# Performance work log

Measured on AMD Instinct MI355X. Metric: run time of the kernel, lower is better.

The kernel has to match this reference:

```python
import jax, jax.numpy as jnp
import numpy as np

N_NODES = 100000

def graph_conv(x, edge_index, w_root, w_rel, b):
    # PyG GraphConv (aggr='add'): out = aggr(x_j) @ W_rel + b + x @ W_root
    src, dst = edge_index[0], edge_index[1]
    msgs = x[src]                                   # [E, F_in] gather
    agg = jax.ops.segment_sum(msgs, dst, num_segments=N_NODES)  # [N, F_in] scatter-add
    return agg @ w_rel + b + x @ w_root             # [N, F_out]


def setup_inputs() -> dict:
    key = jax.random.key(0)
    ks = jax.random.split(key, 12)
    E = 1600000
    return {
        "x": jax.random.normal(ks[0], (N_NODES, 16), dtype=jnp.float32),
        "edge_index": jax.random.randint(ks[1], (2, E), 0, N_NODES, dtype=jnp.int64),
        "w_root1": jax.random.normal(ks[2], (16, 32), dtype=jnp.float32) * 0.1,
        "w_rel1": jax.random.normal(ks[3], (16, 32), dtype=jnp.float32) * 0.1,
        "b1": jax.random.normal(ks[4], (32,), dtype=jnp.float32) * 0.1,
        "w_root2": jax.random.normal(ks[5], (32, 64), dtype=jnp.float32) * 0.1,
        "w_rel2": jax.random.normal(ks[6], (32, 64), dtype=jnp.float32) * 0.1,
        "b2": jax.random.normal(ks[7], (64,), dtype=jnp.float32) * 0.1,
        "fc1_w": jax.random.normal(ks[8], (64, 32), dtype=jnp.float32) * 0.1,
        "fc1_b": jax.random.normal(ks[9], (32,), dtype=jnp.float32) * 0.1,
        "fc2_w": jax.random.normal(ks[10], (32, 16), dtype=jnp.float32) * 0.1,
        "fc2_b": jax.random.normal(ks[11], (16,), dtype=jnp.float32) * 0.1,
    }


def reference(x, edge_index, w_root1, w_rel1, b1, w_root2, w_rel2, b2,
              fc1_w, fc1_b, fc2_w, fc2_b):
    h = jax.nn.relu(graph_conv(x, edge_index, w_root1, w_rel1, b1))   # [N, 32]
    h = jax.nn.relu(graph_conv(h, edge_index, w_root2, w_rel2, b2))   # [N, 64]
    h = jax.nn.relu(h @ fc1_w + fc1_b)                                 # [N, 32]
    return h @ fc2_w + fc2_b                                           # [N, 16]
```

## Files before the change

### kernel.cpp

```cpp
#include <hip/hip_runtime.h>

#define F4E(v,i) ((i)==0?(v).x:((i)==1?(v).y:((i)==2?(v).z:(v).w)))

#define CHUNK 8192

__device__ inline float4 shfl4b(float4 v, int src) {
    float4 r;
    r.x = __shfl(v.x, src, 4); r.y = __shfl(v.y, src, 4);
    r.z = __shfl(v.z, src, 4); r.w = __shfl(v.w, src, 4);
    return r;
}

__global__ __launch_bounds__(512) void k_bhist(
    const int* __restrict__ ei, int* __restrict__ bhist, int E, int NB)
{
    __shared__ int cnt[512];
    int t = threadIdx.x;
    cnt[t] = 0;
    __syncthreads();
    int base = blockIdx.x * CHUNK;
#pragma unroll
    for (int i = 0; i < 16; ++i) {
        int e = base + i * 512 + t;
        if (e < E) {
            int dst = ei[E + e];
            atomicAdd(&cnt[dst >> 8], 1);
        }
    }
    __syncthreads();
    if (t < NB && cnt[t]) atomicAdd(&bhist[t], cnt[t]);
}

__global__ __launch_bounds__(512) void k_bscan(
    const int* __restrict__ bhist, int* __restrict__ bstart,
    int* __restrict__ gcursor, int NB, int E)
{
    __shared__ int s[512];
    int t = threadIdx.x;
    int v0 = (t < NB) ? bhist[t] : 0;
    s[t] = v0;
    __syncthreads();
    for (int off = 1; off < 512; off <<= 1) {
        int v = (t >= off) ? s[t - off] : 0;
        __syncthreads();
        s[t] += v;
        __syncthreads();
    }
    if (t < NB) { int ex = s[t] - v0; bstart[t] = ex; gcursor[t] = ex; }
    if (t == 0) bstart[NB] = E;
}

__global__ __launch_bounds__(512) void k_partition(
    const int* __restrict__ ei, int* __restrict__ gcursor,
    int* __restrict__ epack, int E)
{
    __shared__ int cnt[512], sc[512], lbase[512], gbase[512], lcnt[512];
    __shared__ int stage[CHUNK];
    __shared__ unsigned short stageb[CHUNK];
    int t = threadIdx.x;
    cnt[t] = 0; lcnt[t] = 0;
    __syncthreads();

    int base = blockIdx.x * CHUNK;
    int pk[16], bb[16];
#pragma unroll
    for (int i = 0; i < 16; ++i) {
        int e = base + i * 512 + t;
        if (e < E) {
            int src = ei[e], dst = ei[E + e];
            pk[i] = (src << 8) | (dst & 255);
            bb[i] = dst >> 8;
            atomicAdd(&cnt[bb[i]], 1);
        } else bb[i] = -1;
    }
    __syncthreads();

    int v0 = cnt[t];
    sc[t] = v0;
    __syncthreads();
    for (int off = 1; off < 512; off <<= 1) {
        int v = (t >= off) ? sc[t - off] : 0;
        __syncthreads();
        sc[t] += v;
        __syncthreads();
    }
    lbase[t] = sc[t] - v0;
    if (v0 > 0) gbase[t] = atomicAdd(&gcursor[t], v0);
    __syncthreads();

#pragma unroll
    for (int i = 0; i < 16; ++i) {
        if (bb[i] >= 0) {
            int loc = atomicAdd(&lcnt[bb[i]], 1);
            int slot = lbase[bb[i]] + loc;
            stage[slot] = pk[i];
            stageb[slot] = (unsigned short)bb[i];
        }
    }
    __syncthreads();

    int m = min(CHUNK, E - base);
#pragma unroll
    for (int i = 0; i < 16; ++i) {
        int slot = i * 512 + t;
        if (slot < m) {
            int b = stageb[slot];
            epack[gbase[b] + (slot - lbase[b])] = stage[slot];
        }
    }
}

__global__ __launch_bounds__(256) void k_sort(
    const int* __restrict__ bstart, const int* __restrict__ epack,
    int* __restrict__ rs, int* __restrict__ esorted, int N, int E)
{
    __shared__ int hist[256], cur[256], sc[256];
    int t = threadIdx.x;
    int b = blockIdx.x;
    int s0 = bstart[b], s1 = bstart[b + 1];
    hist[t] = 0;
    __syncthreads();
    for (int e = s0 + t; e < s1; e += 256)
        atomicAdd(&hist[epack[e] & 255], 1);
    __syncthreads();

    int v0 = hist[t];
    sc[t] = v0;
    __syncthreads();
    for (int off = 1; off < 256; off <<= 1) {
        int v = (t >= off) ? sc[t - off] : 0;
        __syncthreads();
        sc[t] += v;
        __syncthreads();
    }
    int excl = sc[t] - v0;
    cur[t] = excl;
    int node = (b << 8) + t;
    if (node < N) rs[node] = s0 + excl;
    if (b == 0 && t == 0) rs[N] = E;
    __syncthreads();

    for (int e = s0 + t; e < s1; e += 256) {
        int pk = epack[e];
        int dlo = pk & 255;
        int pos = s0 + atomicAdd(&cur[dlo], 1);
        esorted[pos] = ((unsigned)pk) >> 8;
    }
}

__global__ __launch_bounds__(256) void k_g1f(
    const float* __restrict__ x, const int* __restrict__ rs,
    const int* __restrict__ esrc,
    const float* __restrict__ wroot, const float* __restrict__ wrel,
    const float* __restrict__ bias, float* __restrict__ h1, int N)
{
    __shared__ float4 s_wr[128], s_wl[128], s_b[8];
    int t = threadIdx.x;
    if (t < 128) {
        s_wr[t] = reinterpret_cast<const float4*>(wroot)[t];
        s_wl[t] = reinterpret_cast<const float4*>(wrel)[t];
    }
    if (t < 8) s_b[t] = reinterpret_cast<const float4*>(bias)[t];
    __syncthreads();

    int tid = blockIdx.x * 256 + t;
    int n = tid >> 2, p = tid & 3;
    if (n >= N) return;
    int s0 = rs[n], s1 = rs[n + 1];
    float4 g = make_float4(0.f, 0.f, 0.f, 0.f);
    int e = s0;
    for (; e + 1 < s1; e += 2) {
        int src0 = esrc[e], src1 = esrc[e + 1];
        float4 v0 = *reinterpret_cast<const float4*>(x + (size_t)src0 * 16 + p * 4);
        float4 v1 = *reinterpret_cast<const float4*>(x + (size_t)src1 * 16 + p * 4);
        g.x += v0.x + v1.x; g.y += v0.y + v1.y;
        g.z += v0.z + v1.z; g.w += v0.w + v1.w;
    }
    if (e < s1) {
        int src0 = esrc[e];
        float4 v0 = *reinterpret_cast<const float4*>(x + (size_t)src0 * 16 + p * 4);
        g.x += v0.x; g.y += v0.y; g.z += v0.z; g.w += v0.w;
    }
    float4 a = *reinterpret_cast<const float4*>(x + (size_t)n * 16 + p * 4);

    int jb = p * 2;
    float4 acc0 = s_b[jb], acc1 = s_b[jb + 1];
#pragma unroll
    for (int kc = 0; kc < 4; ++kc) {
        float4 a4 = shfl4b(a, kc);
        float4 g4 = shfl4b(g, kc);
#pragma unroll
        for (int kk = 0; kk < 4; ++kk) {
            float av = F4E(a4, kk), gv = F4E(g4, kk);
            int k = kc * 4 + kk;
            float4 wr0 = s_wr[k * 8 + jb], wr1 = s_wr[k * 8 + jb + 1];
            float4 wl0 = s_wl[k * 8 + jb], wl1 = s_wl[k * 8 + jb + 1];
            acc0.x += av * wr0.x + gv * wl0.x;
            acc0.y += av * wr0.y + gv * wl0.y;
            acc0.z += av * wr0.z + gv * wl0.z;
            acc0.w += av * wr0.w + gv * wl0.w;
            acc1.x += av * wr1.x + gv * wl1.x;
            acc1.y += av * wr1.y + gv * wl1.y;
            acc1.z += av * wr1.z + gv * wl1.z;
            acc1.w += av * wr1.w + gv * wl1.w;
        }
    }
    acc0.x = fmaxf(acc0.x, 0.f); acc0.y = fmaxf(acc0.y, 0.f);
    acc0.z = fmaxf(acc0.z, 0.f); acc0.w = fmaxf(acc0.w, 0.f);
    acc1.x = fmaxf(acc1.x, 0.f); acc1.y = fmaxf(acc1.y, 0.f);
    acc1.z = fmaxf(acc1.z, 0.f); acc1.w = fmaxf(acc1.w, 0.f);
    float4* o = reinterpret_cast<float4*>(h1 + (size_t)n * 32 + p * 8);
    o[0] = acc0; o[1] = acc1;
}

__global__ __launch_bounds__(256) void k_gather32(
    const float* __restrict__ x, const int* __restrict__ rs,
    const int* __restrict__ esrc, float* __restrict__ agg, int N)
{
    int tid = blockIdx.x * 256 + threadIdx.x;
    int n = tid >> 3, p = tid & 7;
    if (n >= N) return;
    int s0 = rs[n], s1 = rs[n + 1];
    float4 acc = make_float4(0.f, 0.f, 0.f, 0.f);
    int e = s0;
    for (; e + 1 < s1; e += 2) {
        int src0 = esrc[e], src1 = esrc[e + 1];
        float4 v0 = *reinterpret_cast<const float4*>(x + (size_t)src0 * 32 + p * 4);
        float4 v1 = *reinterpret_cast<const float4*>(x + (size_t)src1 * 32 + p * 4);
        acc.x += v0.x + v1.x; acc.y += v0.y + v1.y;
        acc.z += v0.z + v1.z; acc.w += v0.w + v1.w;
    }
    if (e < s1) {
        int src0 = esrc[e];
        float4 v0 = *reinterpret_cast<const float4*>(x + (size_t)src0 * 32 + p * 4);
        acc.x += v0.x; acc.y += v0.y; acc.z += v0.z; acc.w += v0.w;
    }
    *reinterpret_cast<float4*>(agg + (size_t)n * 32 + p * 4) = acc;
}

__global__ __launch_bounds__(256) void k_l2v2(
    const float* __restrict__ h1, const float* __restrict__ agg,
    const float* __restrict__ wroot, const float* __restrict__ wrel,
    const float* __restrict__ bias,
    const float* __restrict__ f1w, const float* __restrict__ f1b,
    const float* __restrict__ f2w, const float* __restrict__ f2b,
    float* __restrict__ out, int N)
{
    __shared__ float4 s_wr[512], s_wl[512], s_b[16];
    __shared__ float4 s_f1[512], s_f2[128], s_b1[8], s_b2[4];
    int t = threadIdx.x;
    for (int i = t; i < 512; i += 256) {
        s_wr[i] = reinterpret_cast<const float4*>(wroot)[i];
        s_wl[i] = reinterpret_cast<const float4*>(wrel)[i];
        s_f1[i] = reinterpret_cast<const float4*>(f1w)[i];
    }
    if (t < 128) s_f2[t] = reinterpret_cast<const float4*>(f2w)[t];
    if (t < 16) s_b[t]  = reinterpret_cast<const float4*>(bias)[t];
    if (t < 8)  s_b1[t] = reinterpret_cast<const float4*>(f1b)[t];
    if (t < 4)  s_b2[t] = reinterpret_cast<const float4*>(f2b)[t];
    __syncthreads();

    int gid = blockIdx.x * 256 + t;
    int n = gid >> 1, p = gid & 1;
    if (n >= N) return;
    const float4* xr = reinterpret_cast<const float4*>(h1 + (size_t)n * 32);
    const float4* ar = reinterpret_cast<const float4*>(agg + (size_t)n * 32);
    float4 X0 = xr[0], X1 = xr[1], X2 = xr[2], X3 = xr[3];
    float4 X4 = xr[4], X5 = xr[5], X6 = xr[6], X7 = xr[7];
    float4 G0 = ar[0], G1 = ar[1], G2 = ar[2], G3 = ar[3];
    float4 G4 = ar[4], G5 = ar[5], G6 = ar[6], G7 = ar[7];

    int jb = p * 8;
    float4 acc[8];
#pragma unroll
    for (int jc = 0; jc < 8; ++jc) acc[jc] = s_b[jb + jc];

#define L2STEP(Xc, Gc, kcv)                                          \
    {                                                                \
        _Pragma("unroll")                                            \
        for (int kk = 0; kk < 4; ++kk) {                             \
            float a = F4E(Xc, kk), g = F4E(Gc, kk);                  \
            int k = (kcv) * 4 + kk;                                  \
            _Pragma("unroll")                                        \
            for (int jc = 0; jc < 8; ++jc) {                         \
                float4 wr = s_wr[k * 16 + jb + jc];                  \
                float4 wl = s_wl[k * 16 + jb + jc];                  \
                acc[jc].x += a * wr.x + g * wl.x;                    \
                acc[jc].y += a * wr.y + g * wl.y;                    \
                acc[jc].z += a * wr.z + g * wl.z;                    \
                acc[jc].w += a * wr.w + g * wl.w;                    \
            }                                                        \
        }                                                            \
    }
    L2STEP(X0, G0, 0) L2STEP(X1, G1, 1) L2STEP(X2, G2, 2) L2STEP(X3, G3, 3)
    L2STEP(X4, G4, 4) L2STEP(X5, G5, 5) L2STEP(X6, G6, 6) L2STEP(X7, G7, 7)
#undef L2STEP

#pragma unroll
    for (int jc = 0; jc < 8; ++jc) {
        acc[jc].x = fmaxf(acc[jc].x, 0.f); acc[jc].y = fmaxf(acc[jc].y, 0.f);
        acc[jc].z = fmaxf(acc[jc].z, 0.f); acc[jc].w = fmaxf(acc[jc].w, 0.f);
    }

    float4 f[8];
    float4 z4 = make_float4(0.f, 0.f, 0.f, 0.f);
#pragma unroll
    for (int jc = 0; jc < 8; ++jc) f[jc] = p ? z4 : s_b1[jc];
#pragma unroll
    for (int kk = 0; kk < 32; ++kk) {
        float hv = F4E(acc[kk >> 2], kk & 3);
        int k = p * 32 + kk;
#pragma unroll
        for (int jc = 0; jc < 8; ++jc) {
            float4 w = s_f1[k * 8 + jc];
            f[jc].x += hv * w.x; f[jc].y += hv * w.y;
            f[jc].z += hv * w.z; f[jc].w += hv * w.w;
        }
    }
#pragma unroll
    for (int jc = 0; jc < 8; ++jc) {
        f[jc].x += __shfl_xor(f[jc].x, 1);
        f[jc].y += __shfl_xor(f[jc].y, 1);
        f[jc].z += __shfl_xor(f[jc].z, 1);
        f[jc].w += __shfl_xor(f[jc].w, 1);
        f[jc].x = fmaxf(f[jc].x, 0.f); f[jc].y = fmaxf(f[jc].y, 0.f);
        f[jc].z = fmaxf(f[jc].z, 0.f); f[jc].w = fmaxf(f[jc].w, 0.f);
    }

    int ob = p * 2;
    float4 o0 = s_b2[ob], o1 = s_b2[ob + 1];
#pragma unroll
    for (int k2 = 0; k2 < 32; ++k2) {
        float a = F4E(f[k2 >> 2], k2 & 3);
        float4 w0 = s_f2[k2 * 4 + ob], w1 = s_f2[k2 * 4 + ob + 1];
        o0.x += a * w0.x; o0.y += a * w0.y; o0.z += a * w0.z; o0.w += a * w0.w;
        o1.x += a * w1.x; o1.y += a * w1.y; o1.z += a * w1.z; o1.w += a * w1.w;
    }
    float4* o = reinterpret_cast<float4*>(out + (size_t)n * 16 + p * 8);
    o[0] = o0; o[1] = o1;
}

extern "C" void kernel_launch(void* const* d_in, const int* in_sizes, int n_in,
                              void* d_out, int out_size, void* d_ws, size_t ws_size,
                              hipStream_t stream)
{
    const float* x   = (const float*)d_in[0];
    const int*   ei  = (const int*)d_in[1];
    const float* wr1 = (const float*)d_in[2];
    const float* wl1 = (const float*)d_in[3];
    const float* b1  = (const float*)d_in[4];
    const float* wr2 = (const float*)d_in[5];
    const float* wl2 = (const float*)d_in[6];
    const float* b2  = (const float*)d_in[7];
    const float* f1w = (const float*)d_in[8];
    const float* f1b = (const float*)d_in[9];
    const float* f2w = (const float*)d_in[10];
    const float* f2b = (const float*)d_in[11];
    float* out = (float*)d_out;

    const int N  = in_sizes[0] / 16;
    const int E  = in_sizes[1] / 2;
    const int NB = (N + 255) >> 8;

    float* ws      = (float*)d_ws;
    float* h1      = ws;
    float* agg2    = ws + (size_t)N * 32;
    int*   esorted = (int*)(ws + (size_t)N * 64);
    int*   epack   = esorted + E;
    int*   rs      = epack + E;
    int*   bhist   = rs + N + 1;
    int*   bstart  = bhist + NB;
    int*   gcursor = bstart + NB + 1;

    hipMemsetAsync(bhist, 0, (size_t)NB * sizeof(int), stream);

    int nchunk = (E + CHUNK - 1) / CHUNK;
    int g_g1 = (N * 4 + 255) / 256;
    int g_g2 = (N * 8 + 255) / 256;
    int g_l2 = (N * 2 + 255) / 256;

    k_bhist    <<<nchunk, 512, 0, stream>>>(ei, bhist, E, NB);
    k_bscan    <<<1,      512, 0, stream>>>(bhist, bstart, gcursor, NB, E);
    k_partition<<<nchunk, 512, 0, stream>>>(ei, gcursor, epack, E);
    k_sort     <<<NB,     256, 0, stream>>>(bstart, epack, rs, esorted, N, E);

    k_g1f      <<<g_g1, 256, 0, stream>>>(x, rs, esorted, wr1, wl1, b1, h1, N);
    k_gather32 <<<g_g2, 256, 0, stream>>>(h1, rs, esorted, agg2, N);
    k_l2v2     <<<g_l2, 256, 0, stream>>>(h1, agg2, wr2, wl2, b2,
                                          f1w, f1b, f2w, f2b, out, N);
}
```

Measured before the change: 232.2 us.

## Fuse layer-2 gather with dense MLP tail and halve partition chunk size

Merges the layer-2 neighbor gather and the dense layer-2/fc1/fc2 kernel into one kernel with 8 threads per node. Each thread gathers a float4 slice of the aggregate, then shares the slices with shuffles for the GraphConv matmul. fc1 partial sums are reduced with an xor-shuffle tree across the 8 lanes, and the fc1 weights are stored in shared memory with a rotated layout to avoid bank conflicts. This removes the agg2 intermediate write and read plus one launch, at the cost of more shuffles and register pressure. Separately, the partition chunk size is halved so those kernels launch more blocks with fewer edges each.

```diff
diff --git a/kernel.cpp b/kernel.cpp
--- a/kernel.cpp
+++ b/kernel.cpp
@@ -2,7 +2,8 @@
 
 #define F4E(v,i) ((i)==0?(v).x:((i)==1?(v).y:((i)==2?(v).z:(v).w)))
 
-#define CHUNK 8192
+#define CHUNK 4096
+#define ITERS 8
 
 __device__ inline float4 shfl4b(float4 v, int src) {
     float4 r;
@@ -10,6 +11,12 @@
     r.z = __shfl(v.z, src, 4); r.w = __shfl(v.w, src, 4);
     return r;
 }
+__device__ inline float4 shfl8b(float4 v, int src) {
+    float4 r;
+    r.x = __shfl(v.x, src, 8); r.y = __shfl(v.y, src, 8);
+    r.z = __shfl(v.z, src, 8); r.w = __shfl(v.w, src, 8);
+    return r;
+}
 
 __global__ __launch_bounds__(512) void k_bhist(
     const int* __restrict__ ei, int* __restrict__ bhist, int E, int NB)
@@ -20,7 +27,7 @@
     __syncthreads();
     int base = blockIdx.x * CHUNK;
 #pragma unroll
-    for (int i = 0; i < 16; ++i) {
+    for (int i = 0; i < ITERS; ++i) {
         int e = base + i * 512 + t;
         if (e < E) {
             int dst = ei[E + e];
@@ -62,9 +69,9 @@
     __syncthreads();
 
     int base = blockIdx.x * CHUNK;
-    int pk[16], bb[16];
-#pragma unroll
-    for (int i = 0; i < 16; ++i) {
+    int pk[ITERS], bb[ITERS];
+#pragma unroll
+    for (int i = 0; i < ITERS; ++i) {
         int e = base + i * 512 + t;
         if (e < E) {
             int src = ei[e], dst = ei[E + e];
@@ -89,7 +96,7 @@
     __syncthreads();
 
 #pragma unroll
-    for (int i = 0; i < 16; ++i) {
+    for (int i = 0; i < ITERS; ++i) {
         if (bb[i] >= 0) {
             int loc = atomicAdd(&lcnt[bb[i]], 1);
             int slot = lbase[bb[i]] + loc;
@@ -101,7 +108,7 @@
 
     int m = min(CHUNK, E - base);
 #pragma unroll
-    for (int i = 0; i < 16; ++i) {
+    for (int i = 0; i < ITERS; ++i) {
         int slot = i * 512 + t;
         if (slot < m) {
             int b = stageb[slot];
@@ -213,33 +220,9 @@
     o[0] = acc0; o[1] = acc1;
 }
 
-__global__ __launch_bounds__(256) void k_gather32(
-    const float* __restrict__ x, const int* __restrict__ rs,
-    const int* __restrict__ esrc, float* __restrict__ agg, int N)
-{
-    int tid = blockIdx.x * 256 + threadIdx.x;
-    int n = tid >> 3, p = tid & 7;
-    if (n >= N) return;
-    int s0 = rs[n], s1 = rs[n + 1];
-    float4 acc = make_float4(0.f, 0.f, 0.f, 0.f);
-    int e = s0;
-    for (; e + 1 < s1; e += 2) {
-        int src0 = esrc[e], src1 = esrc[e + 1];
-        float4 v0 = *reinterpret_cast<const float4*>(x + (size_t)src0 * 32 + p * 4);
-        float4 v1 = *reinterpret_cast<const float4*>(x + (size_t)src1 * 32 + p * 4);
-        acc.x += v0.x + v1.x; acc.y += v0.y + v1.y;
-        acc.z += v0.z + v1.z; acc.w += v0.w + v1.w;
-    }
-    if (e < s1) {
-        int src0 = esrc[e];
-        float4 v0 = *reinterpret_cast<const float4*>(x + (size_t)src0 * 32 + p * 4);
-        acc.x += v0.x; acc.y += v0.y; acc.z += v0.z; acc.w += v0.w;
-    }
-    *reinterpret_cast<float4*>(agg + (size_t)n * 32 + p * 4) = acc;
-}
-
-__global__ __launch_bounds__(256) void k_l2v2(
-    const float* __restrict__ h1, const float* __restrict__ agg,
+__global__ __launch_bounds__(256) void k_g2f(
+    const float* __restrict__ h1, const int* __restrict__ rs,
+    const int* __restrict__ esrc,
     const float* __restrict__ wroot, const float* __restrict__ wrel,
     const float* __restrict__ bias,
     const float* __restrict__ f1w, const float* __restrict__ f1b,
@@ -247,97 +230,112 @@
     float* __restrict__ out, int N)
 {
     __shared__ float4 s_wr[512], s_wl[512], s_b[16];
-    __shared__ float4 s_f1[512], s_f2[128], s_b1[8], s_b2[4];
+    __shared__ float4 s_f1[512];
+    __shared__ float  s_f2[512];
+    __shared__ float4 s_b1[8];
+    __shared__ float  s_b2[16];
     int t = threadIdx.x;
     for (int i = t; i < 512; i += 256) {
         s_wr[i] = reinterpret_cast<const float4*>(wroot)[i];
         s_wl[i] = reinterpret_cast<const float4*>(wrel)[i];
-        s_f1[i] = reinterpret_cast<const float4*>(f1w)[i];
-    }
-    if (t < 128) s_f2[t] = reinterpret_cast<const float4*>(f2w)[t];
+        int k = i >> 3, jc = i & 7;
+        s_f1[(i & ~7) | ((jc + (k >> 3)) & 7)] = reinterpret_cast<const float4*>(f1w)[i];
+        s_f2[i] = f2w[i];
+    }
     if (t < 16) s_b[t]  = reinterpret_cast<const float4*>(bias)[t];
     if (t < 8)  s_b1[t] = reinterpret_cast<const float4*>(f1b)[t];
-    if (t < 4)  s_b2[t] = reinterpret_cast<const float4*>(f2b)[t];
-    __syncthreads();
-
-    int gid = blockIdx.x * 256 + t;
-    int n = gid >> 1, p = gid & 1;
+    if (t < 16) s_b2[t] = f2b[t];
+    __syncthreads();
+
+    int tid = blockIdx.x * 256 + t;
+    int n = tid >> 3, p = tid & 7;
     if (n >= N) return;
-    const float4* xr = reinterpret_cast<const float4*>(h1 + (size_t)n * 32);
-    const float4* ar = reinterpret_cast<const float4*>(agg + (size_t)n * 32);
-    float4 X0 = xr[0], X1 = xr[1], X2 = xr[2], X3 = xr[3];
-    float4 X4 = xr[4], X5 = xr[5], X6 = xr[6], X7 = xr[7];
-    float4 G0 = ar[0], G1 = ar[1], G2 = ar[2], G3 = ar[3];
-    float4 G4 = ar[4], G5 = ar[5], G6 = ar[6], G7 = ar[7];
-
-    int jb = p * 8;
-    float4 acc[8];
-#pragma unroll
-    for (int jc = 0; jc < 8; ++jc) acc[jc] = s_b[jb + jc];
-
-#define L2STEP(Xc, Gc, kcv)                                          \
-    {                                                                \
-        _Pragma("unroll")                                            \
-        for (int kk = 0; kk < 4; ++kk) {                             \
-            float a = F4E(Xc, kk), g = F4E(Gc, kk);                  \
-            int k = (kcv) * 4 + kk;                                  \
-            _Pragma("unroll")                                        \
-            for (int jc = 0; jc < 8; ++jc) {                         \
-                float4 wr = s_wr[k * 16 + jb + jc];                  \
-                float4 wl = s_wl[k * 16 + jb + jc];                  \
-                acc[jc].x += a * wr.x + g * wl.x;                    \
-                acc[jc].y += a * wr.y + g * wl.y;                    \
-                acc[jc].z += a * wr.z + g * wl.z;                    \
-                acc[jc].w += a * wr.w + g * wl.w;                    \
-            }                                                        \
-        }                                                            \
-    }
-    L2STEP(X0, G0, 0) L2STEP(X1, G1, 1) L2STEP(X2, G2, 2) L2STEP(X3, G3, 3)
-    L2STEP(X4, G4, 4) L2STEP(X5, G5, 5) L2STEP(X6, G6, 6) L2STEP(X7, G7, 7)
-#undef L2STEP
-
-#pragma unroll
-    for (int jc = 0; jc < 8; ++jc) {
-        acc[jc].x = fmaxf(acc[jc].x, 0.f); acc[jc].y = fmaxf(acc[jc].y, 0.f);
-        acc[jc].z = fmaxf(acc[jc].z, 0.f); acc[jc].w = fmaxf(acc[jc].w, 0.f);
-    }
+
+    int s0 = rs[n], s1 = rs[n + 1];
+    float4 g = make_float4(0.f, 0.f, 0.f, 0.f);
+    int e = s0;
+    for (; e + 1 < s1; e += 2) {
+        int src0 = esrc[e], src1 = esrc[e + 1];
+        float4 v0 = *reinterpret_cast<const float4*>(h1 + (size_t)src0 * 32 + p * 4);
+        float4 v1 = *reinterpret_cast<const float4*>(h1 + (size_t)src1 * 32 + p * 4);
+        g.x += v0.x + v1.x; g.y += v0.y + v1.y;
+        g.z += v0.z + v1.z; g.w += v0.w + v1.w;
+    }
+    if (e < s1) {
+        int src0 = esrc[e];
+        float4 v0 = *reinterpret_cast<const float4*>(h1 + (size_t)src0 * 32 + p * 4);
+        g.x += v0.x; g.y += v0.y; g.z += v0.z; g.w += v0.w;
+    }
+    float4 a = *reinterpret_cast<const float4*>(h1 + (size_t)n * 32 + p * 4);
+
+    int jb = p * 2;
+    float4 acc0 = s_b[jb], acc1 = s_b[jb + 1];
+#pragma unroll
+    for (int kc = 0; kc < 8; ++kc) {
+        float4 a4 = shfl8b(a, kc);
+        float4 g4 = shfl8b(g, kc);
+#pragma unroll
+        for (int kk = 0; kk < 4; ++kk) {
+            float av = F4E(a4, kk), gv = F4E(g4, kk);
+            int k = kc * 4 + kk;
+            float4 wr0 = s_wr[k * 16 + jb], wr1 = s_wr[k * 16 + jb + 1];
+            float4 wl0 = s_wl[k * 16 + jb], wl1 = s_wl[k * 16 + jb + 1];
+            acc0.x += av * wr0.x + gv * wl0.x;
+            acc0.y += av * wr0.y + gv * wl0.y;
+            acc0.z += av * wr0.z + gv * wl0.z;
+            acc0.w += av * wr0.w + gv * wl0.w;
+            acc1.x += av * wr1.x + gv * wl1.x;
+            acc1.y += av * wr1.y + gv * wl1.y;
+            acc1.z += av * wr1.z + gv * wl1.z;
+            acc1.w += av * wr1.w + gv * wl1.w;
+        }
+    }
+    acc0.x = fmaxf(acc0.x, 0.f); acc0.y = fmaxf(acc0.y, 0.f);
+    acc0.z = fmaxf(acc0.z, 0.f); acc0.w = fmaxf(acc0.w, 0.f);
+    acc1.x = fmaxf(acc1.x, 0.f); acc1.y = fmaxf(acc1.y, 0.f);
+    acc1.z = fmaxf(acc1.z, 0.f); acc1.w = fmaxf(acc1.w, 0.f);
 
     float4 f[8];
     float4 z4 = make_float4(0.f, 0.f, 0.f, 0.f);
 #pragma unroll
     for (int jc = 0; jc < 8; ++jc) f[jc] = p ? z4 : s_b1[jc];
 #pragma unroll
-    for (int kk = 0; kk < 32; ++kk) {
-        float hv = F4E(acc[kk >> 2], kk & 3);
-        int k = p * 32 + kk;
+    for (int kk = 0; kk < 8; ++kk) {
+        float hv = (kk < 4) ? F4E(acc0, kk) : F4E(acc1, kk - 4);
+        int k = p * 8 + kk;
+        int row = k * 8;
 #pragma unroll
         for (int jc = 0; jc < 8; ++jc) {
-            float4 w = s_f1[k * 8 + jc];
+            float4 w = s_f1[row | ((jc + p) & 7)];
             f[jc].x += hv * w.x; f[jc].y += hv * w.y;
             f[jc].z += hv * w.z; f[jc].w += hv * w.w;
         }
     }
 #pragma unroll
+    for (int m = 1; m < 8; m <<= 1) {
+#pragma unroll
+        for (int jc = 0; jc < 8; ++jc) {
+            f[jc].x += __shfl_xor(f[jc].x, m);
+            f[jc].y += __shfl_xor(f[jc].y, m);
+            f[jc].z += __shfl_xor(f[jc].z, m);
+            f[jc].w += __shfl_xor(f[jc].w, m);
+        }
+    }
+#pragma unroll
     for (int jc = 0; jc < 8; ++jc) {
-        f[jc].x += __shfl_xor(f[jc].x, 1);
-        f[jc].y += __shfl_xor(f[jc].y, 1);
-        f[jc].z += __shfl_xor(f[jc].z, 1);
-        f[jc].w += __shfl_xor(f[jc].w, 1);
         f[jc].x = fmaxf(f[jc].x, 0.f); f[jc].y = fmaxf(f[jc].y, 0.f);
         f[jc].z = fmaxf(f[jc].z, 0.f); f[jc].w = fmaxf(f[jc].w, 0.f);
     }
 
-    int ob = p * 2;
-    float4 o0 = s_b2[ob], o1 = s_b2[ob + 1];
+    float o0 = s_b2[p * 2], o1 = s_b2[p * 2 + 1];
 #pragma unroll
     for (int k2 = 0; k2 < 32; ++k2) {
-        float a = F4E(f[k2 >> 2], k2 & 3);
-        float4 w0 = s_f2[k2 * 4 + ob], w1 = s_f2[k2 * 4 + ob + 1];
-        o0.x += a * w0.x; o0.y += a * w0.y; o0.z += a * w0.z; o0.w += a * w0.w;
-        o1.x += a * w1.x; o1.y += a * w1.y; o1.z += a * w1.z; o1.w += a * w1.w;
-    }
-    float4* o = reinterpret_cast<float4*>(out + (size_t)n * 16 + p * 8);
-    o[0] = o0; o[1] = o1;
+        float av = F4E(f[k2 >> 2], k2 & 3);
+        o0 += av * s_f2[k2 * 16 + p * 2];
+        o1 += av * s_f2[k2 * 16 + p * 2 + 1];
+    }
+    float2* o = reinterpret_cast<float2*>(out + (size_t)n * 16 + p * 2);
+    *o = make_float2(o0, o1);
 }
 
 extern "C" void kernel_launch(void* const* d_in, const int* in_sizes, int n_in,
@@ -364,8 +362,7 @@
 
     float* ws      = (float*)d_ws;
     float* h1      = ws;
-    float* agg2    = ws + (size_t)N * 32;
-    int*   esorted = (int*)(ws + (size_t)N * 64);
+    int*   esorted = (int*)(ws + (size_t)N * 32);
     int*   epack   = esorted + E;
     int*   rs      = epack + E;
     int*   bhist   = rs + N + 1;
@@ -377,7 +374,6 @@
     int nchunk = (E + CHUNK - 1) / CHUNK;
     int g_g1 = (N * 4 + 255) / 256;
     int g_g2 = (N * 8 + 255) / 256;
-    int g_l2 = (N * 2 + 255) / 256;
 
     k_bhist    <<<nchunk, 512, 0, stream>>>(ei, bhist, E, NB);
     k_bscan    <<<1,      512, 0, stream>>>(bhist, bstart, gcursor, NB, E);
@@ -385,7 +381,6 @@
     k_sort     <<<NB,     256, 0, stream>>>(bstart, epack, rs, esorted, N, E);
 
     k_g1f      <<<g_g1, 256, 0, stream>>>(x, rs, esorted, wr1, wl1, b1, h1, N);
-    k_gather32 <<<g_g2, 256, 0, stream>>>(h1, rs, esorted, agg2, N);
-    k_l2v2     <<<g_l2, 256, 0, stream>>>(h1, agg2, wr2, wl2, b2,
+    k_g2f      <<<g_g2, 256, 0, stream>>>(h1, rs, esorted, wr2, wl2, b2,
                                           f1w, f1b, f2w, f2b, out, N);
 }
```

After: 229.5 us. Within noise of the previous version (-1.2%).
